# Optimization experiments

Hardware: AMD Instinct MI355X
Metric: run time of the kernel (lower is better)

## Reference

```python
import jax, jax.numpy as jnp
import numpy as np

NUM_HEADS = 12


def setup_inputs() -> dict:
    key = jax.random.key(0)
    k1, k2, k3 = jax.random.split(key, 3)
    B, N, C = 2, 2048, 768
    x = jax.random.normal(k1, (B, N, C), dtype=jnp.float32)
    # xavier_uniform-ish scaled weights
    w_qkv = jax.random.normal(k2, (C, 3 * C), dtype=jnp.float32) * (1.0 / np.sqrt(C))
    w_proj = jax.random.normal(k3, (C, C), dtype=jnp.float32) * (1.0 / np.sqrt(C))
    b_proj = jnp.zeros((C,), dtype=jnp.float32)
    return {"x": x, "w_qkv": w_qkv, "w_proj": w_proj, "b_proj": b_proj}


def reference(x, w_qkv, w_proj, b_proj):
    B, N, C = x.shape
    H = NUM_HEADS
    D = C // H
    scale = D ** -0.5
    # [B, N, 3, H, D]
    qkv = (x @ w_qkv).reshape(B, N, 3, H, D)
    q = qkv[:, :, 0].transpose(0, 2, 1, 3)  # [B, H, N, D]
    k = qkv[:, :, 1].transpose(0, 2, 1, 3)
    v = qkv[:, :, 2].transpose(0, 2, 1, 3)
    attn = jnp.einsum("bhnd,bhmd->bhnm", q, k) * scale  # [B, H, N, N]
    attn = jax.nn.softmax(attn, axis=-1)  # attn_drop = 0.0 -> identity
    out = jnp.einsum("bhnm,bhmd->bhnd", attn, v)  # [B, H, N, D]
    out = out.transpose(0, 2, 1, 3).reshape(B, N, C)
    return out @ w_proj + b_proj  # proj_drop = 0.0 -> identity
```

## Files before the change

kernel.cpp:

```cpp
#include <hip/hip_runtime.h>
#include <hip/hip_bf16.h>

typedef __attribute__((ext_vector_type(8))) short short8;
typedef __attribute__((ext_vector_type(4))) float f32x4;
typedef __attribute__((ext_vector_type(4))) int int4v;

#define HD 64
#define NH 12
#define SEQ 2048
#define CDIM 768
#define NT (SEQ / 64)

#define QSCALE 0.180336880f

static __device__ __forceinline__ unsigned short f2bf(float f) {
    __hip_bfloat16 h = __float2bfloat16(f);
    return __builtin_bit_cast(unsigned short, h);
}

static __device__ __forceinline__ unsigned cvtpk_bf16(float a, float b) {
    unsigned r;
    asm("v_cvt_pk_bf16_f32 %0, %1, %2" : "=v"(r) : "v"(a), "v"(b));
    return r;
}

#define GLDS16(gp, lp) __builtin_amdgcn_global_load_lds( \
    (const __attribute__((address_space(1))) void*)(gp), \
    (__attribute__((address_space(3))) void*)(lp), 16, 0, 0)

static __device__ __forceinline__ int kperm_f(int r) {
    const int kt = r >> 4, gg = (r >> 2) & 3, jj = r & 3;
    return 32 * (kt & 1) + 8 * gg + 4 * (kt >> 1) + jj;
}

static __device__ __forceinline__ void transpose_tile(const float* __restrict__ in,
        unsigned short* __restrict__ out, int K, int C, int bx, int by,
        float (*t)[33], int tid) {
    const int k0 = bx * 32, c0 = by * 32;
    const int r = tid >> 3, c4 = (tid & 7) * 4;
    const float4 v = *reinterpret_cast<const float4*>(in + (size_t)(k0 + r) * C + c0 + c4);
    t[r][c4 + 0] = v.x; t[r][c4 + 1] = v.y; t[r][c4 + 2] = v.z; t[r][c4 + 3] = v.w;
    __syncthreads();
    ushort4 o;
    o.x = f2bf(t[c4 + 0][r]); o.y = f2bf(t[c4 + 1][r]);
    o.z = f2bf(t[c4 + 2][r]); o.w = f2bf(t[c4 + 3][r]);
    *reinterpret_cast<ushort4*>(out + (size_t)(c0 + r) * K + k0 + c4) = o;
}

__global__ __launch_bounds__(256) void prep_kernel(
        const float* __restrict__ x, const float* __restrict__ wq, const float* __restrict__ wp,
        unsigned short* __restrict__ xb, unsigned short* __restrict__ wqt, unsigned short* __restrict__ wpt) {
    __shared__ float t[32][33];
    const int blk = blockIdx.x, tid = threadIdx.x;
    if (blk < 1728) {
        transpose_tile(wq, wqt, 768, 2304, blk % 24, blk / 24, t, tid);
    } else if (blk < 2304) {
        const int b2 = blk - 1728;
        transpose_tile(wp, wpt, 768, 768, b2 % 24, b2 / 24, t, tid);
    } else {
        const int b3 = blk - 2304;
        #pragma unroll
        for (int it = 0; it < 4; it++) {
            const int i = (b3 * 4 + it) * 256 + tid;
            const float4 v = reinterpret_cast<const float4*>(x)[i];
            ushort4 o;
            o.x = f2bf(v.x); o.y = f2bf(v.y); o.z = f2bf(v.z); o.w = f2bf(v.w);
            reinterpret_cast<ushort4*>(xb)[i] = o;
        }
    }
}

template<int EPI, int BM>
__global__ __launch_bounds__(256, 3) void gemm_kernel(
    const unsigned short* __restrict__ A,
    const unsigned short* __restrict__ Bt,
    const int K, const int N,
    unsigned short* __restrict__ Qo, unsigned short* __restrict__ Ko, unsigned short* __restrict__ Vo,
    float* __restrict__ Cout, const float* __restrict__ bias)
{
    constexpr int MF = (BM == 128) ? 4 : 2;
    const int tid = threadIdx.x;
    const int wave = tid >> 6, lane = tid & 63;
    const int g = lane >> 4, li = lane & 15;
    const int wr = wave >> 1, wc = wave & 1;
    const int m0 = blockIdx.x * BM, n0 = blockIdx.y * 128;

    __shared__ short As[3][BM * 32];
    __shared__ short Bs[3][128 * 32];

    f32x4 acc[MF][4];
    #pragma unroll
    for (int i = 0; i < MF; i++)
        #pragma unroll
        for (int j = 0; j < 4; j++)
            acc[i][j] = (f32x4){0.f, 0.f, 0.f, 0.f};

    const int srow = wave * 16 + (lane >> 2);
    const int scol = (lane & 3) * 8;
    const unsigned short* aSrc = A + (size_t)(m0 + srow) * K + scol;
    const unsigned short* bSrc = Bt + (size_t)(n0 + srow) * K + scol;
    const int d0 = wave * 16 * 32, d1 = (wave * 16 + 64) * 32;
    const size_t rowskip = (size_t)64 * K;

    #define GSTAGE(kk, bb) do { \
        GLDS16(aSrc + (kk) * 32,           &As[bb][d0]); \
        if (BM == 128) GLDS16(aSrc + (kk) * 32 + rowskip, &As[bb][d1]); \
        GLDS16(bSrc + (kk) * 32,           &Bs[bb][d0]); \
        GLDS16(bSrc + (kk) * 32 + rowskip, &Bs[bb][d1]); \
    } while (0)

    #define GWAIT_DEEP do { \
        if (BM == 128) asm volatile("s_waitcnt vmcnt(4)\n\ts_barrier" ::: "memory"); \
        else           asm volatile("s_waitcnt vmcnt(3)\n\ts_barrier" ::: "memory"); \
    } while (0)

    const int nk = K >> 5;
    GSTAGE(0, 0);
    GSTAGE(1, 1);
    GWAIT_DEEP;

    int cur = 0;
    for (int kk = 0; kk < nk; ++kk) {
        const int sbuf = (cur == 0) ? 2 : cur - 1;
        const bool stage = (kk + 2 < nk);
        if (stage) GSTAGE(kk + 2, sbuf);
        const short* Ab = As[cur];
        const short* Bb = Bs[cur];
        short8 af[MF], bfr[4];
        #pragma unroll
        for (int mf = 0; mf < MF; mf++)
            af[mf] = *reinterpret_cast<const short8*>(&Ab[(wr * (BM / 2) + mf * 16 + li) * 32 + 8 * g]);
        #pragma unroll
        for (int nf = 0; nf < 4; nf++)
            bfr[nf] = *reinterpret_cast<const short8*>(&Bb[(wc * 64 + nf * 16 + li) * 32 + 8 * g]);
        __builtin_amdgcn_s_setprio(1);
        #pragma unroll
        for (int mf = 0; mf < MF; mf++)
            #pragma unroll
            for (int nf = 0; nf < 4; nf++)
                acc[mf][nf] = __builtin_amdgcn_mfma_f32_16x16x32_bf16(af[mf], bfr[nf], acc[mf][nf], 0, 0, 0);
        __builtin_amdgcn_s_setprio(0);
        if (stage) GWAIT_DEEP;
        else       asm volatile("s_waitcnt vmcnt(0)\n\ts_barrier" ::: "memory");
        cur = (cur == 2) ? 0 : cur + 1;
    }
    #undef GSTAGE
    #undef GWAIT_DEEP

    #pragma unroll
    for (int mf = 0; mf < MF; mf++) {
        #pragma unroll
        for (int nf = 0; nf < 4; nf++) {
            #pragma unroll
            for (int j = 0; j < 4; j++) {
                const int r = m0 + wr * (BM / 2) + mf * 16 + 4 * g + j;
                const int c = n0 + wc * 64 + nf * 16 + li;
                const float v = acc[mf][nf][j];
                if (EPI == 0) {
                    const int s = c / 768, rem = c % 768;
                    const int hh = rem >> 6, d = rem & 63;
                    const int bb = r >> 11, n = r & (SEQ - 1);
                    if (s == 0)
                        Qo[(((size_t)bb * NH + hh) * SEQ + n) * HD + d] = f2bf(v * QSCALE);
                    else if (s == 1)
                        Ko[(((size_t)bb * NH + hh) * SEQ + n) * HD + d] = f2bf(v);
                    else
                        Vo[(((size_t)bb * NH + hh) * HD + d) * SEQ + n] = f2bf(v);
                } else {
                    Cout[(size_t)r * N + c] = v + bias[c];
                }
            }
        }
    }
}


static __device__ __forceinline__ void qk_mfma(
    f32x4 (&s)[4], const short* kb, int sl0, int sl1, int li,
    const short8 qf0, const short8 qf1)
{
    #pragma unroll
    for (int kt = 0; kt < 4; kt++) s[kt] = (f32x4){0.f, 0.f, 0.f, 0.f};
    __builtin_amdgcn_s_setprio(1);
    #pragma unroll
    for (int kt = 0; kt < 4; kt++) {
        const short8 ka0 = *reinterpret_cast<const short8*>(&kb[(16 * kt + li) * 64 + sl0]);
        const short8 ka1 = *reinterpret_cast<const short8*>(&kb[(16 * kt + li) * 64 + sl1]);
        s[kt] = __builtin_amdgcn_mfma_f32_16x16x32_bf16(ka0, qf0, s[kt], 0, 0, 0);
        s[kt] = __builtin_amdgcn_mfma_f32_16x16x32_bf16(ka1, qf1, s[kt], 0, 0, 0);
    }
    __builtin_amdgcn_s_setprio(0);
}

static __device__ __forceinline__ void sm_pv(
    const f32x4 (&s)[4], const short* vb, int sl0, int sl1, int li,
    const short8 ones, f32x4 (&o_acc)[4], f32x4& l_acc)
{
    float p[4][4];
    #pragma unroll
    for (int kt = 0; kt < 4; kt++)
        #pragma unroll
        for (int j = 0; j < 4; j++)
            p[kt][j] = __builtin_amdgcn_exp2f(s[kt][j]);

    const int4v i0 = { (int)cvtpk_bf16(p[0][0], p[0][1]), (int)cvtpk_bf16(p[0][2], p[0][3]),
                       (int)cvtpk_bf16(p[2][0], p[2][1]), (int)cvtpk_bf16(p[2][2], p[2][3]) };
    const int4v i1 = { (int)cvtpk_bf16(p[1][0], p[1][1]), (int)cvtpk_bf16(p[1][2], p[1][3]),
                       (int)cvtpk_bf16(p[3][0], p[3][1]), (int)cvtpk_bf16(p[3][2], p[3][3]) };
    const short8 pa0 = __builtin_bit_cast(short8, i0);
    const short8 pa1 = __builtin_bit_cast(short8, i1);

    __builtin_amdgcn_s_setprio(1);
    l_acc = __builtin_amdgcn_mfma_f32_16x16x32_bf16(ones, pa0, l_acc, 0, 0, 0);
    l_acc = __builtin_amdgcn_mfma_f32_16x16x32_bf16(ones, pa1, l_acc, 0, 0, 0);
    #pragma unroll
    for (int nf = 0; nf < 4; nf++) {
        const short8 va0 = *reinterpret_cast<const short8*>(&vb[(16 * nf + li) * 64 + sl0]);
        const short8 va1 = *reinterpret_cast<const short8*>(&vb[(16 * nf + li) * 64 + sl1]);
        o_acc[nf] = __builtin_amdgcn_mfma_f32_16x16x32_bf16(va0, pa0, o_acc[nf], 0, 0, 0);
        o_acc[nf] = __builtin_amdgcn_mfma_f32_16x16x32_bf16(va1, pa1, o_acc[nf], 0, 0, 0);
    }
    __builtin_amdgcn_s_setprio(0);
}

__global__ __launch_bounds__(256, 3) void attn_kernel(
    const unsigned short* __restrict__ Q,
    const unsigned short* __restrict__ Kg,
    const unsigned short* __restrict__ Vtg,
    unsigned short* __restrict__ O)
{
    const int tid = threadIdx.x;
    const int wave = tid >> 6, lane = tid & 63;
    const int g = lane >> 4, li = lane & 15;
    const int head = blockIdx.y;
    const int b = head / NH, h = head % NH;
    const int q0 = blockIdx.x * 64 + wave * 16;
    const size_t plane = (size_t)head * SEQ * HD;

    __shared__ short Ks[2][64 * 64];
    __shared__ short Vs[3][64 * 64];

    short8 qf0, qf1;
    {
        const unsigned short* qp = Q + plane + (size_t)(q0 + li) * HD + 8 * g;
        qf0 = *reinterpret_cast<const short8*>(qp);
        qf1 = *reinterpret_cast<const short8*>(qp + 32);
    }
    const short8 ones = {0x3F80, 0x3F80, 0x3F80, 0x3F80, 0x3F80, 0x3F80, 0x3F80, 0x3F80};

    const int lr = lane >> 3;
    const int colS = ((lane & 7) ^ lr) * 8;
    const int rA = wave * 16 + lr;
    const int rB = rA + 8;
    const unsigned short* kSrcA = Kg + plane + (size_t)kperm_f(rA) * HD + colS;
    const unsigned short* kSrcB = Kg + plane + (size_t)kperm_f(rB) * HD + colS;
    const unsigned short* vSrcA = Vtg + plane + (size_t)rA * SEQ + colS;
    const unsigned short* vSrcB = Vtg + plane + (size_t)rB * SEQ + colS;
    const int stA = wave * 1024, stB = stA + 512;

    #define STAGE(kv, kbuf, vdst) do { \
        GLDS16(kSrcA + (size_t)(kv) * HD, &Ks[kbuf][stA]); \
        GLDS16(kSrcB + (size_t)(kv) * HD, &Ks[kbuf][stB]); \
        GLDS16(vSrcA + (kv),              (vdst) + stA); \
        GLDS16(vSrcB + (kv),              (vdst) + stB); \
    } while (0)

    f32x4 o_acc[4], l_acc;
    #pragma unroll
    for (int nf = 0; nf < 4; nf++) o_acc[nf] = (f32x4){0.f, 0.f, 0.f, 0.f};
    l_acc = (f32x4){0.f, 0.f, 0.f, 0.f};

    const int sl0 = (g ^ (li & 7)) * 8;
    const int sl1 = ((g + 4) ^ (li & 7)) * 8;

    short* vbP = &Vs[2][0];
    short* vbC = &Vs[0][0];
    short* vbN = &Vs[1][0];

    f32x4 sA[4], sB[4];

    STAGE(0, 0, vbC);
    asm volatile("s_waitcnt vmcnt(0)\n\ts_barrier" ::: "memory");

    #define ITER(IT, SC, SP, DOP) do { \
        if ((IT) + 1 < NT) STAGE(((IT) + 1) * 64, ((IT) + 1) & 1, vbN); \
        qk_mfma(SC, &Ks[(IT) & 1][0], sl0, sl1, li, qf0, qf1); \
        if (DOP) sm_pv(SP, vbP, sl0, sl1, li, ones, o_acc, l_acc); \
        asm volatile("s_waitcnt vmcnt(0)\n\ts_barrier" ::: "memory"); \
        { short* t_ = vbP; vbP = vbC; vbC = vbN; vbN = t_; } \
    } while (0)

    for (int pr = 0; pr < NT / 2; ++pr) {
        ITER(pr * 2,     sA, sB, pr > 0);
        ITER(pr * 2 + 1, sB, sA, true);
    }
    #undef ITER
    #undef STAGE

    sm_pv(sB, vbP, sl0, sl1, li, ones, o_acc, l_acc);

    const float inv = 1.0f / l_acc[0];
    unsigned short* dst = O + ((size_t)b * SEQ + q0 + li) * CDIM + h * HD + 4 * g;
    #pragma unroll
    for (int nf = 0; nf < 4; nf++) {
        ushort4 o;
        o.x = f2bf(o_acc[nf][0] * inv);
        o.y = f2bf(o_acc[nf][1] * inv);
        o.z = f2bf(o_acc[nf][2] * inv);
        o.w = f2bf(o_acc[nf][3] * inv);
        *reinterpret_cast<ushort4*>(dst + 16 * nf) = o;
    }
}

extern "C" void kernel_launch(void* const* d_in, const int* in_sizes, int n_in,
                              void* d_out, int out_size, void* d_ws, size_t ws_size,
                              hipStream_t stream) {
    const float* x      = (const float*)d_in[0];
    const float* w_qkv  = (const float*)d_in[1];
    const float* w_proj = (const float*)d_in[2];
    const float* b_proj = (const float*)d_in[3];
    float* out = (float*)d_out;

    char* p = (char*)d_ws;
    auto take = [&](size_t bytes) { char* r = p; p += (bytes + 255) & ~(size_t)255; return r; };
    unsigned short* xb      = (unsigned short*)take((size_t)4096 * 768 * 2);
    unsigned short* wqkv_t  = (unsigned short*)take((size_t)2304 * 768 * 2);
    unsigned short* wproj_t = (unsigned short*)take((size_t)768 * 768 * 2);
    unsigned short* Qb      = (unsigned short*)take((size_t)24 * 2048 * 64 * 2);
    unsigned short* Kb      = (unsigned short*)take((size_t)24 * 2048 * 64 * 2);
    unsigned short* Vb      = (unsigned short*)take((size_t)24 * 2048 * 64 * 2);
    unsigned short* Ob      = (unsigned short*)take((size_t)4096 * 768 * 2);

    prep_kernel<<<3072, 256, 0, stream>>>(x, w_qkv, w_proj, xb, wqkv_t, wproj_t);
    gemm_kernel<0, 64><<<dim3(64, 18), 256, 0, stream>>>(xb, wqkv_t, 768, 2304, Qb, Kb, Vb, nullptr, nullptr);
    attn_kernel<<<dim3(32, 24), 256, 0, stream>>>(Qb, Kb, Vb, Ob);
    gemm_kernel<1, 64><<<dim3(64, 6), 256, 0, stream>>>(Ob, wproj_t, 768, 768, nullptr, nullptr, nullptr, out, b_proj);
}
```

Measured before the change: 103.7 us.

## Process two query tiles per wave in attention, halving waves per block

Each attention wave now handles 32 query rows as two 16-row tiles, so every K/V fragment read from shared memory feeds twice as many MFMAs. Blocks shrink from 4 waves to 2 and each wave stages twice as many K/V rows. The launch bounds change from (256,3) to (128,1), which raises the register budget but may cut occupancy and latency hiding. The QKV GEMM launch also switches to its 128-row tile variant with half the blocks.

```diff
diff --git a/kernel.cpp b/kernel.cpp
--- a/kernel.cpp
+++ b/kernel.cpp
@@ -175,19 +175,24 @@
 }
 
 
-static __device__ __forceinline__ void qk_mfma(
-    f32x4 (&s)[4], const short* kb, int sl0, int sl1, int li,
-    const short8 qf0, const short8 qf1)
+static __device__ __forceinline__ void qk2_mfma(
+    f32x4 (&sa)[4], f32x4 (&sb)[4], const short* kb, int sl0, int sl1, int li,
+    const short8 qA0, const short8 qA1, const short8 qB0, const short8 qB1)
 {
     #pragma unroll
-    for (int kt = 0; kt < 4; kt++) s[kt] = (f32x4){0.f, 0.f, 0.f, 0.f};
+    for (int kt = 0; kt < 4; kt++) {
+        sa[kt] = (f32x4){0.f, 0.f, 0.f, 0.f};
+        sb[kt] = (f32x4){0.f, 0.f, 0.f, 0.f};
+    }
     __builtin_amdgcn_s_setprio(1);
     #pragma unroll
     for (int kt = 0; kt < 4; kt++) {
         const short8 ka0 = *reinterpret_cast<const short8*>(&kb[(16 * kt + li) * 64 + sl0]);
         const short8 ka1 = *reinterpret_cast<const short8*>(&kb[(16 * kt + li) * 64 + sl1]);
-        s[kt] = __builtin_amdgcn_mfma_f32_16x16x32_bf16(ka0, qf0, s[kt], 0, 0, 0);
-        s[kt] = __builtin_amdgcn_mfma_f32_16x16x32_bf16(ka1, qf1, s[kt], 0, 0, 0);
+        sa[kt] = __builtin_amdgcn_mfma_f32_16x16x32_bf16(ka0, qA0, sa[kt], 0, 0, 0);
+        sa[kt] = __builtin_amdgcn_mfma_f32_16x16x32_bf16(ka1, qA1, sa[kt], 0, 0, 0);
+        sb[kt] = __builtin_amdgcn_mfma_f32_16x16x32_bf16(ka0, qB0, sb[kt], 0, 0, 0);
+        sb[kt] = __builtin_amdgcn_mfma_f32_16x16x32_bf16(ka1, qB1, sb[kt], 0, 0, 0);
     }
     __builtin_amdgcn_s_setprio(0);
 }
@@ -223,7 +228,7 @@
     __builtin_amdgcn_s_setprio(0);
 }
 
-__global__ __launch_bounds__(256, 3) void attn_kernel(
+__global__ __launch_bounds__(128, 1) void attn_kernel(
     const unsigned short* __restrict__ Q,
     const unsigned short* __restrict__ Kg,
     const unsigned short* __restrict__ Vtg,
@@ -234,41 +239,55 @@
     const int g = lane >> 4, li = lane & 15;
     const int head = blockIdx.y;
     const int b = head / NH, h = head % NH;
-    const int q0 = blockIdx.x * 64 + wave * 16;
+    const int qw = blockIdx.x * 64 + wave * 32;
     const size_t plane = (size_t)head * SEQ * HD;
 
     __shared__ short Ks[2][64 * 64];
     __shared__ short Vs[3][64 * 64];
 
-    short8 qf0, qf1;
+    short8 qA0, qA1, qB0, qB1;
     {
-        const unsigned short* qp = Q + plane + (size_t)(q0 + li) * HD + 8 * g;
-        qf0 = *reinterpret_cast<const short8*>(qp);
-        qf1 = *reinterpret_cast<const short8*>(qp + 32);
+        const unsigned short* qp = Q + plane + (size_t)(qw + li) * HD + 8 * g;
+        qA0 = *reinterpret_cast<const short8*>(qp);
+        qA1 = *reinterpret_cast<const short8*>(qp + 32);
+        const unsigned short* qp2 = qp + (size_t)16 * HD;
+        qB0 = *reinterpret_cast<const short8*>(qp2);
+        qB1 = *reinterpret_cast<const short8*>(qp2 + 32);
     }
     const short8 ones = {0x3F80, 0x3F80, 0x3F80, 0x3F80, 0x3F80, 0x3F80, 0x3F80, 0x3F80};
 
     const int lr = lane >> 3;
     const int colS = ((lane & 7) ^ lr) * 8;
-    const int rA = wave * 16 + lr;
-    const int rB = rA + 8;
-    const unsigned short* kSrcA = Kg + plane + (size_t)kperm_f(rA) * HD + colS;
-    const unsigned short* kSrcB = Kg + plane + (size_t)kperm_f(rB) * HD + colS;
-    const unsigned short* vSrcA = Vtg + plane + (size_t)rA * SEQ + colS;
-    const unsigned short* vSrcB = Vtg + plane + (size_t)rB * SEQ + colS;
-    const int stA = wave * 1024, stB = stA + 512;
+    const int r0 = wave * 32 + lr, r1 = r0 + 8, r2 = r0 + 16, r3 = r0 + 24;
+    const unsigned short* kS0 = Kg + plane + (size_t)kperm_f(r0) * HD + colS;
+    const unsigned short* kS1 = Kg + plane + (size_t)kperm_f(r1) * HD + colS;
+    const unsigned short* kS2 = Kg + plane + (size_t)kperm_f(r2) * HD + colS;
+    const unsigned short* kS3 = Kg + plane + (size_t)kperm_f(r3) * HD + colS;
+    const unsigned short* vS0 = Vtg + plane + (size_t)r0 * SEQ + colS;
+    const unsigned short* vS1 = Vtg + plane + (size_t)r1 * SEQ + colS;
+    const unsigned short* vS2 = Vtg + plane + (size_t)r2 * SEQ + colS;
+    const unsigned short* vS3 = Vtg + plane + (size_t)r3 * SEQ + colS;
+    const int st0 = wave * 2048, st1 = st0 + 512, st2 = st0 + 1024, st3 = st0 + 1536;
 
     #define STAGE(kv, kbuf, vdst) do { \
-        GLDS16(kSrcA + (size_t)(kv) * HD, &Ks[kbuf][stA]); \
-        GLDS16(kSrcB + (size_t)(kv) * HD, &Ks[kbuf][stB]); \
-        GLDS16(vSrcA + (kv),              (vdst) + stA); \
-        GLDS16(vSrcB + (kv),              (vdst) + stB); \
+        GLDS16(kS0 + (size_t)(kv) * HD, &Ks[kbuf][st0]); \
+        GLDS16(kS1 + (size_t)(kv) * HD, &Ks[kbuf][st1]); \
+        GLDS16(kS2 + (size_t)(kv) * HD, &Ks[kbuf][st2]); \
+        GLDS16(kS3 + (size_t)(kv) * HD, &Ks[kbuf][st3]); \
+        GLDS16(vS0 + (kv),              (vdst) + st0); \
+        GLDS16(vS1 + (kv),              (vdst) + st1); \
+        GLDS16(vS2 + (kv),              (vdst) + st2); \
+        GLDS16(vS3 + (kv),              (vdst) + st3); \
     } while (0)
 
-    f32x4 o_acc[4], l_acc;
-    #pragma unroll
-    for (int nf = 0; nf < 4; nf++) o_acc[nf] = (f32x4){0.f, 0.f, 0.f, 0.f};
-    l_acc = (f32x4){0.f, 0.f, 0.f, 0.f};
+    f32x4 oA[4], oB[4], lA, lB;
+    #pragma unroll
+    for (int nf = 0; nf < 4; nf++) {
+        oA[nf] = (f32x4){0.f, 0.f, 0.f, 0.f};
+        oB[nf] = (f32x4){0.f, 0.f, 0.f, 0.f};
+    }
+    lA = (f32x4){0.f, 0.f, 0.f, 0.f};
+    lB = (f32x4){0.f, 0.f, 0.f, 0.f};
 
     const int sl0 = (g ^ (li & 7)) * 8;
     const int sl1 = ((g + 4) ^ (li & 7)) * 8;
@@ -277,38 +296,57 @@
     short* vbC = &Vs[0][0];
     short* vbN = &Vs[1][0];
 
-    f32x4 sA[4], sB[4];
+    f32x4 sAa[4], sAb[4], sBa[4], sBb[4];
 
     STAGE(0, 0, vbC);
     asm volatile("s_waitcnt vmcnt(0)\n\ts_barrier" ::: "memory");
 
-    #define ITER(IT, SC, SP, DOP) do { \
+    #define ITER(IT, SCa, SCb, SPa, SPb, DOP) do { \
         if ((IT) + 1 < NT) STAGE(((IT) + 1) * 64, ((IT) + 1) & 1, vbN); \
-        qk_mfma(SC, &Ks[(IT) & 1][0], sl0, sl1, li, qf0, qf1); \
-        if (DOP) sm_pv(SP, vbP, sl0, sl1, li, ones, o_acc, l_acc); \
+        qk2_mfma(SCa, SCb, &Ks[(IT) & 1][0], sl0, sl1, li, qA0, qA1, qB0, qB1); \
+        if (DOP) { \
+            sm_pv(SPa, vbP, sl0, sl1, li, ones, oA, lA); \
+            sm_pv(SPb, vbP, sl0, sl1, li, ones, oB, lB); \
+        } \
         asm volatile("s_waitcnt vmcnt(0)\n\ts_barrier" ::: "memory"); \
         { short* t_ = vbP; vbP = vbC; vbC = vbN; vbN = t_; } \
     } while (0)
 
     for (int pr = 0; pr < NT / 2; ++pr) {
-        ITER(pr * 2,     sA, sB, pr > 0);
-        ITER(pr * 2 + 1, sB, sA, true);
+        ITER(pr * 2,     sAa, sAb, sBa, sBb, pr > 0);
+        ITER(pr * 2 + 1, sBa, sBb, sAa, sAb, true);
     }
     #undef ITER
     #undef STAGE
 
-    sm_pv(sB, vbP, sl0, sl1, li, ones, o_acc, l_acc);
-
-    const float inv = 1.0f / l_acc[0];
-    unsigned short* dst = O + ((size_t)b * SEQ + q0 + li) * CDIM + h * HD + 4 * g;
-    #pragma unroll
-    for (int nf = 0; nf < 4; nf++) {
-        ushort4 o;
-        o.x = f2bf(o_acc[nf][0] * inv);
-        o.y = f2bf(o_acc[nf][1] * inv);
-        o.z = f2bf(o_acc[nf][2] * inv);
-        o.w = f2bf(o_acc[nf][3] * inv);
-        *reinterpret_cast<ushort4*>(dst + 16 * nf) = o;
+    sm_pv(sBa, vbP, sl0, sl1, li, ones, oA, lA);
+    sm_pv(sBb, vbP, sl0, sl1, li, ones, oB, lB);
+
+    {
+        const float inv = 1.0f / lA[0];
+        unsigned short* dst = O + ((size_t)b * SEQ + qw + li) * CDIM + h * HD + 4 * g;
+        #pragma unroll
+        for (int nf = 0; nf < 4; nf++) {
+            ushort4 o;
+            o.x = f2bf(oA[nf][0] * inv);
+            o.y = f2bf(oA[nf][1] * inv);
+            o.z = f2bf(oA[nf][2] * inv);
+            o.w = f2bf(oA[nf][3] * inv);
+            *reinterpret_cast<ushort4*>(dst + 16 * nf) = o;
+        }
+    }
+    {
+        const float inv = 1.0f / lB[0];
+        unsigned short* dst = O + ((size_t)b * SEQ + qw + 16 + li) * CDIM + h * HD + 4 * g;
+        #pragma unroll
+        for (int nf = 0; nf < 4; nf++) {
+            ushort4 o;
+            o.x = f2bf(oB[nf][0] * inv);
+            o.y = f2bf(oB[nf][1] * inv);
+            o.z = f2bf(oB[nf][2] * inv);
+            o.w = f2bf(oB[nf][3] * inv);
+            *reinterpret_cast<ushort4*>(dst + 16 * nf) = o;
+        }
     }
 }
 
@@ -332,7 +370,7 @@
     unsigned short* Ob      = (unsigned short*)take((size_t)4096 * 768 * 2);
 
     prep_kernel<<<3072, 256, 0, stream>>>(x, w_qkv, w_proj, xb, wqkv_t, wproj_t);
-    gemm_kernel<0, 64><<<dim3(64, 18), 256, 0, stream>>>(xb, wqkv_t, 768, 2304, Qb, Kb, Vb, nullptr, nullptr);
-    attn_kernel<<<dim3(32, 24), 256, 0, stream>>>(Qb, Kb, Vb, Ob);
+    gemm_kernel<0, 128><<<dim3(32, 18), 256, 0, stream>>>(xb, wqkv_t, 768, 2304, Qb, Kb, Vb, nullptr, nullptr);
+    attn_kernel<<<dim3(32, 24), 128, 0, stream>>>(Qb, Kb, Vb, Ob);
     gemm_kernel<1, 64><<<dim3(64, 6), 256, 0, stream>>>(Ob, wproj_t, 768, 768, nullptr, nullptr, nullptr, out, b_proj);
 }
```

Result: no change. 105.5 us (+1.8%).
